# Kernel tuning notes

Hardware: AMD Instinct MI355X
Metric: run time of the kernel (lower is better)

Reference implementation:

```python
import jax, jax.numpy as jnp
import numpy as np

N_NODES = 50000
N_EDGES = 640000
IN_CH = 128
OUT_CH = 128
HID = 2 * OUT_CH  # 256


def _glorot(key, shape):
    fan_in, fan_out = shape
    lim = np.sqrt(6.0 / (fan_in + fan_out)).astype(np.float32)
    return jax.random.uniform(key, shape, jnp.float32, -lim, lim)


def setup_inputs() -> dict:
    key = jax.random.key(0)
    ks = jax.random.split(key, 8)
    x = jax.random.normal(ks[0], (N_NODES, IN_CH), jnp.float32)
    edge_index = jax.random.randint(ks[1], (2, N_EDGES), 0, N_NODES, jnp.int64)
    # SAGEConv layer 1: lin_l (neighbor branch, with bias), lin_r (root branch, no bias)
    w1_l = _glorot(ks[2], (IN_CH, HID))
    b1_l = jnp.zeros((HID,), jnp.float32)
    w1_r = _glorot(ks[3], (IN_CH, HID))
    # SAGEConv layer 2
    w2_l = _glorot(ks[4], (HID, OUT_CH))
    b2_l = jnp.zeros((OUT_CH,), jnp.float32)
    w2_r = _glorot(ks[5], (HID, OUT_CH))
    return {"x": x, "edge_index": edge_index,
            "w1_l": w1_l, "b1_l": b1_l, "w1_r": w1_r,
            "w2_l": w2_l, "b2_l": b2_l, "w2_r": w2_r}


def _sage_conv(x, src, dst, w_l, b_l, w_r):
    # mean aggregation of source-node features onto destination nodes
    msgs = x[src]                                       # [E, C] gather
    agg = jax.ops.segment_sum(msgs, dst, num_segments=N_NODES)  # [N, C]
    cnt = jax.ops.segment_sum(jnp.ones((src.shape[0],), x.dtype), dst,
                              num_segments=N_NODES)     # [N]
    mean = agg / jnp.maximum(cnt, 1.0)[:, None]
    # out = lin_l(mean_neighbors) + lin_r(x_root)
    return mean @ w_l + b_l + x @ w_r


def reference(x, edge_index, w1_l, b1_l, w1_r, w2_l, b2_l, w2_r):
    src, dst = edge_index[0], edge_index[1]
    h = _sage_conv(x, src, dst, w1_l, b1_l, w1_r)
    h = jax.nn.relu(h)
    return _sage_conv(h, src, dst, w2_l, b2_l, w2_r)
```

## Files before the change

### kernel.cpp

```cpp
#include <hip/hip_runtime.h>

#define N_NODES 50000
#define N_EDGES 640000
#define IN_CH 128
#define OUT_CH 128
#define HID 256
#define M_PAD 50048
#define NBLK ((N_NODES + 255) / 256)

typedef unsigned int uint;
typedef unsigned short ushort;

__device__ __forceinline__ ushort f2b(float f) {
    uint u = __float_as_uint(f);
    u += 0x7FFFu + ((u >> 16) & 1u);
    return (ushort)(u >> 16);
}
__device__ __forceinline__ float b2f_lo(uint u) { return __uint_as_float(u << 16); }
__device__ __forceinline__ float b2f_hi(uint u) { return __uint_as_float(u & 0xFFFF0000u); }
__device__ __forceinline__ uint packb(float lo, float hi) {
    return (uint)f2b(lo) | ((uint)f2b(hi) << 16);
}

__device__ __forceinline__ void gload_lds16(const ushort* g, ushort* l) {
    __builtin_amdgcn_global_load_lds(
        (const __attribute__((address_space(1))) void*)g,
        (__attribute__((address_space(3))) void*)l, 16, 0, 0);
}

__global__ __launch_bounds__(256) void count_deg(const int* __restrict__ dst,
                                                 int* __restrict__ deg) {
    int e = blockIdx.x * blockDim.x + threadIdx.x;
    if (e < N_EDGES) atomicAdd(&deg[dst[e]], 1);
}

__global__ __launch_bounds__(256) void block_sums(const int* __restrict__ deg,
                                                  int* __restrict__ bsum) {
    __shared__ int tmp[256];
    int i = blockIdx.x * 256 + threadIdx.x;
    tmp[threadIdx.x] = (i < N_NODES) ? deg[i] : 0;
    __syncthreads();
    for (int off = 128; off > 0; off >>= 1) {
        if (threadIdx.x < off) tmp[threadIdx.x] += tmp[threadIdx.x + off];
        __syncthreads();
    }
    if (threadIdx.x == 0) bsum[blockIdx.x] = tmp[0];
}

__global__ __launch_bounds__(256) void scan_bsums(int* __restrict__ bsum,
                                                  int* __restrict__ rowptr) {
    __shared__ int tmp[256];
    int i = threadIdx.x;
    int v = (i < NBLK) ? bsum[i] : 0;
    tmp[i] = v;
    __syncthreads();
    for (int off = 1; off < 256; off <<= 1) {
        int t = (i >= off) ? tmp[i - off] : 0;
        __syncthreads();
        tmp[i] += t;
        __syncthreads();
    }
    if (i < NBLK) bsum[i] = tmp[i] - v;
    if (i == 0) rowptr[N_NODES] = N_EDGES;
}

__global__ __launch_bounds__(256) void scan_final(const int* __restrict__ deg,
                                                  const int* __restrict__ bsum,
                                                  int* __restrict__ rowptr) {
    __shared__ int tmp[256];
    int i = blockIdx.x * 256 + threadIdx.x;
    int v = (i < N_NODES) ? deg[i] : 0;
    tmp[threadIdx.x] = v;
    __syncthreads();
    for (int off = 1; off < 256; off <<= 1) {
        int t = (threadIdx.x >= off) ? tmp[threadIdx.x - off] : 0;
        __syncthreads();
        tmp[threadIdx.x] += t;
        __syncthreads();
    }
    if (i < N_NODES) rowptr[i] = bsum[blockIdx.x] + tmp[threadIdx.x] - v;
}

__global__ __launch_bounds__(256) void fill_csr(const int* __restrict__ src,
                                                const int* __restrict__ dst,
                                                const int* __restrict__ rowptr,
                                                int* __restrict__ cursor,
                                                int* __restrict__ col) {
    int e = blockIdx.x * blockDim.x + threadIdx.x;
    if (e >= N_EDGES) return;
    int d = dst[e];
    int p = atomicAdd(&cursor[d], 1);
    col[rowptr[d] + p] = src[e];
}

__global__ __launch_bounds__(256) void cast_all(
    const float* __restrict__ x, const float* __restrict__ w1l,
    const float* __restrict__ w1r, const float* __restrict__ w2l,
    const float* __restrict__ w2r, ushort* __restrict__ xcat,
    ushort* __restrict__ w1f, ushort* __restrict__ w2f) {
    int id = blockIdx.x * 256 + threadIdx.x;
    if (id < 800000) {
        long long base = (long long)id * 8;
        float4 a = *(const float4*)(x + base);
        float4 b = *(const float4*)(x + base + 4);
        uint4 o;
        o.x = packb(a.x, a.y);
        o.y = packb(a.z, a.w);
        o.z = packb(b.x, b.y);
        o.w = packb(b.z, b.w);
        int row = id >> 4;
        int c = id & 15;
        ((uint4*)xcat)[(size_t)row * 32 + 16 + c] = o;
    } else if (id < 865536) {
        int i = id - 800000;
        int n0 = i >> 12, kk = (i >> 9) & 7, lane = (i >> 3) & 63, j = i & 7;
        int n = n0 * 16 + (lane & 15);
        int k = kk * 32 + (lane >> 4) * 8 + j;
        float v = (k < 128) ? w1l[k * 256 + n] : w1r[(k - 128) * 256 + n];
        w1f[i] = f2b(v);
    } else {
        int i = id - 865536;
        int n0 = i >> 12, kk = (i >> 9) & 7, lane = (i >> 3) & 63, j = i & 7;
        int n = n0 * 16 + (lane & 15);
        int k = kk * 32 + (lane >> 4) * 8 + j;
        float v = (n < 128) ? w2l[k * 128 + n] : w2r[k * 128 + (n - 128)];
        w2f[i] = f2b(v);
    }
}

__global__ __launch_bounds__(256) void aggregate_mean1(
    const int* __restrict__ rowptr, const int* __restrict__ col,
    ushort* __restrict__ xcat) {
    int t = blockIdx.x * 256 + threadIdx.x;
    int node = t >> 5;
    int q = t & 15;
    int half = (t >> 4) & 1;
    if (node >= N_NODES) return;
    int beg = rowptr[node], end = rowptr[node + 1];
    float acc[8] = {0.f, 0.f, 0.f, 0.f, 0.f, 0.f, 0.f, 0.f};
    const uint4* f4 = (const uint4*)xcat;
    for (int j = beg + half; j < end; j += 2) {
        int s = col[j];
        uint4 v = f4[(size_t)s * 32 + 16 + q];
        acc[0] += b2f_lo(v.x); acc[1] += b2f_hi(v.x);
        acc[2] += b2f_lo(v.y); acc[3] += b2f_hi(v.y);
        acc[4] += b2f_lo(v.z); acc[5] += b2f_hi(v.z);
        acc[6] += b2f_lo(v.w); acc[7] += b2f_hi(v.w);
    }
#pragma unroll
    for (int k = 0; k < 8; ++k) acc[k] += __shfl_xor(acc[k], 16);
    if (half == 0) {
        float inv = 1.0f / fmaxf((float)(end - beg), 1.0f);
        uint4 o;
        o.x = packb(acc[0] * inv, acc[1] * inv);
        o.y = packb(acc[2] * inv, acc[3] * inv);
        o.z = packb(acc[4] * inv, acc[5] * inv);
        o.w = packb(acc[6] * inv, acc[7] * inv);
        ((uint4*)xcat)[(size_t)node * 32 + q] = o;
    }
}

__global__ __launch_bounds__(256) void combine2(
    const ushort* __restrict__ hw, const int* __restrict__ rowptr,
    const int* __restrict__ col, const float* __restrict__ bias,
    float* __restrict__ out) {
    int t = blockIdx.x * 256 + threadIdx.x;
    int node = t >> 5;
    int q = t & 15;
    int half = (t >> 4) & 1;
    if (node >= N_NODES) return;
    int beg = rowptr[node], end = rowptr[node + 1];
    float acc[8] = {0.f, 0.f, 0.f, 0.f, 0.f, 0.f, 0.f, 0.f};
    const uint4* f4 = (const uint4*)hw;
    for (int j = beg + half; j < end; j += 2) {
        int s = col[j];
        uint4 v = f4[(size_t)s * 32 + q];
        acc[0] += b2f_lo(v.x); acc[1] += b2f_hi(v.x);
        acc[2] += b2f_lo(v.y); acc[3] += b2f_hi(v.y);
        acc[4] += b2f_lo(v.z); acc[5] += b2f_hi(v.z);
        acc[6] += b2f_lo(v.w); acc[7] += b2f_hi(v.w);
    }
#pragma unroll
    for (int k = 0; k < 8; ++k) acc[k] += __shfl_xor(acc[k], 16);
    if (half == 0) {
        float inv = 1.0f / fmaxf((float)(end - beg), 1.0f);
        uint4 r = f4[(size_t)node * 32 + 16 + q];
        float4 b0 = *(const float4*)(bias + q * 8);
        float4 b1 = *(const float4*)(bias + q * 8 + 4);
        float4 o0, o1;
        o0.x = acc[0] * inv + b2f_lo(r.x) + b0.x;
        o0.y = acc[1] * inv + b2f_hi(r.x) + b0.y;
        o0.z = acc[2] * inv + b2f_lo(r.y) + b0.z;
        o0.w = acc[3] * inv + b2f_hi(r.y) + b0.w;
        o1.x = acc[4] * inv + b2f_lo(r.z) + b1.x;
        o1.y = acc[5] * inv + b2f_hi(r.z) + b1.y;
        o1.z = acc[6] * inv + b2f_lo(r.w) + b1.z;
        o1.w = acc[7] * inv + b2f_hi(r.w) + b1.w;
        *(float4*)(out + (size_t)node * 128 + q * 8) = o0;
        *(float4*)(out + (size_t)node * 128 + q * 8 + 4) = o1;
    }
}

using bf16x8 = __attribute__((ext_vector_type(8))) short;
using f32x4  = __attribute__((ext_vector_type(4))) float;

__global__ __launch_bounds__(256) void fused_gemm(
    const ushort* __restrict__ A, const ushort* __restrict__ w1f,
    const ushort* __restrict__ w2f, const float* __restrict__ b1,
    ushort* __restrict__ hw) {
    __shared__ alignas(16) ushort As[64 * 128];
    __shared__ alignas(16) ushort hS[64 * 256];

    const int tid = threadIdx.x;
    const int lane = tid & 63;
    const int wave = tid >> 6;
    const int quad = lane >> 4;
    const int l16 = lane & 15;
    const int bm = blockIdx.x * 64;

    const int srow = tid >> 4;
    const int sslot = tid & 15;

    f32x4 acc[4][4];
#pragma unroll
    for (int rt = 0; rt < 4; ++rt)
#pragma unroll
        for (int ct = 0; ct < 4; ++ct) acc[rt][ct] = (f32x4){0.f, 0.f, 0.f, 0.f};

#pragma unroll
    for (int kh = 0; kh < 2; ++kh) {
#pragma unroll
        for (int r = 0; r < 4; ++r) {
            int rl = r * 16 + srow;
            int c = sslot ^ (rl & 7);
            const ushort* g = A + (size_t)(bm + rl) * 256 + kh * 128 + c * 8;
            gload_lds16(g, &As[rl * 128 + sslot * 8]);
        }
        __syncthreads();
#pragma unroll
        for (int kk = 0; kk < 128; kk += 32) {
            bf16x8 af[4];
#pragma unroll
            for (int rt = 0; rt < 4; ++rt) {
                int row = rt * 16 + l16;
                int slot = ((kk >> 3) + quad) ^ (row & 7);
                af[rt] = *(const bf16x8*)&As[row * 128 + slot * 8];
            }
            int kkidx = kh * 4 + (kk >> 5);
#pragma unroll
            for (int ct = 0; ct < 4; ++ct) {
                int n0 = wave * 4 + ct;
                bf16x8 bf = *(const bf16x8*)(w1f + (((size_t)(n0 * 8 + kkidx) * 64 + lane) << 3));
                acc[0][ct] = __builtin_amdgcn_mfma_f32_16x16x32_bf16(af[0], bf, acc[0][ct], 0, 0, 0);
                acc[1][ct] = __builtin_amdgcn_mfma_f32_16x16x32_bf16(af[1], bf, acc[1][ct], 0, 0, 0);
                acc[2][ct] = __builtin_amdgcn_mfma_f32_16x16x32_bf16(af[2], bf, acc[2][ct], 0, 0, 0);
                acc[3][ct] = __builtin_amdgcn_mfma_f32_16x16x32_bf16(af[3], bf, acc[3][ct], 0, 0, 0);
            }
        }
        __syncthreads();
    }

#pragma unroll
    for (int ct = 0; ct < 4; ++ct) {
        int colg = wave * 64 + ct * 16 + l16;
        float bv = b1[colg];
        int c_chunk = colg >> 3;
        int off = colg & 7;
#pragma unroll
        for (int rt = 0; rt < 4; ++rt) {
#pragma unroll
            for (int reg = 0; reg < 4; ++reg) {
                int row = rt * 16 + quad * 4 + reg;
                float v = fmaxf(acc[rt][ct][reg] + bv, 0.0f);
                int slot = c_chunk ^ (row & 7);
                hS[row * 256 + slot * 8 + off] = f2b(v);
            }
        }
    }
    __syncthreads();

#pragma unroll
    for (int rt = 0; rt < 4; ++rt)
#pragma unroll
        for (int ct = 0; ct < 4; ++ct) acc[rt][ct] = (f32x4){0.f, 0.f, 0.f, 0.f};

#pragma unroll
    for (int kk = 0; kk < 256; kk += 32) {
        bf16x8 af[4];
#pragma unroll
        for (int rt = 0; rt < 4; ++rt) {
            int row = rt * 16 + l16;
            int slot = ((kk >> 3) + quad) ^ (row & 7);
            af[rt] = *(const bf16x8*)&hS[row * 256 + slot * 8];
        }
        int kkidx = kk >> 5;
#pragma unroll
        for (int ct = 0; ct < 4; ++ct) {
            int n0 = wave * 4 + ct;
            bf16x8 bf = *(const bf16x8*)(w2f + (((size_t)(n0 * 8 + kkidx) * 64 + lane) << 3));
            acc[0][ct] = __builtin_amdgcn_mfma_f32_16x16x32_bf16(af[0], bf, acc[0][ct], 0, 0, 0);
            acc[1][ct] = __builtin_amdgcn_mfma_f32_16x16x32_bf16(af[1], bf, acc[1][ct], 0, 0, 0);
            acc[2][ct] = __builtin_amdgcn_mfma_f32_16x16x32_bf16(af[2], bf, acc[2][ct], 0, 0, 0);
            acc[3][ct] = __builtin_amdgcn_mfma_f32_16x16x32_bf16(af[3], bf, acc[3][ct], 0, 0, 0);
        }
    }
    __syncthreads();

#pragma unroll
    for (int ct = 0; ct < 4; ++ct) {
        int colg = wave * 64 + ct * 16 + l16;
        int c_chunk = colg >> 3;
        int off = colg & 7;
#pragma unroll
        for (int rt = 0; rt < 4; ++rt) {
#pragma unroll
            for (int reg = 0; reg < 4; ++reg) {
                int row = rt * 16 + quad * 4 + reg;
                int slot = c_chunk ^ (row & 7);
                hS[row * 256 + slot * 8 + off] = f2b(acc[rt][ct][reg]);
            }
        }
    }
    __syncthreads();
#pragma unroll
    for (int r = 0; r < 8; ++r) {
        int row = r * 8 + (tid >> 5);
        int chunk = tid & 31;
        int slot = chunk ^ (row & 7);
        uint4 v = *(const uint4*)&hS[row * 256 + slot * 8];
        *(uint4*)(hw + (size_t)(bm + row) * 256 + chunk * 8) = v;
    }
}

extern "C" void kernel_launch(void* const* d_in, const int* in_sizes, int n_in,
                              void* d_out, int out_size, void* d_ws, size_t ws_size,
                              hipStream_t stream) {
    const float* x    = (const float*)d_in[0];
    const int*   ei   = (const int*)d_in[1];
    const float* w1_l = (const float*)d_in[2];
    const float* b1_l = (const float*)d_in[3];
    const float* w1_r = (const float*)d_in[4];
    const float* w2_l = (const float*)d_in[5];
    const float* b2_l = (const float*)d_in[6];
    const float* w2_r = (const float*)d_in[7];
    float* out = (float*)d_out;

    const int* src = ei;
    const int* dst = ei + N_EDGES;

    int* deg    = (int*)d_ws;
    int* cursor = deg + N_NODES;
    int* rowptr = cursor + N_NODES;
    int* bsum   = rowptr + (N_NODES + 1);
    int* col    = bsum + NBLK;
    size_t int_bytes = (size_t)(2 * N_NODES + (N_NODES + 1) + NBLK + N_EDGES) * 4;
    size_t ofs = (int_bytes + 15) & ~(size_t)15;
    ushort* xcat = (ushort*)((char*)d_ws + ofs);
    ushort* hw   = xcat + (size_t)M_PAD * HID;
    ushort* w1f  = hw + (size_t)M_PAD * HID;
    ushort* w2f  = w1f + HID * HID;

    hipMemsetAsync(deg, 0, 2 * (size_t)N_NODES * sizeof(int), stream);

    count_deg<<<(N_EDGES + 255) / 256, 256, 0, stream>>>(dst, deg);
    block_sums<<<NBLK, 256, 0, stream>>>(deg, bsum);
    scan_bsums<<<1, 256, 0, stream>>>(bsum, rowptr);
    scan_final<<<NBLK, 256, 0, stream>>>(deg, bsum, rowptr);
    fill_csr<<<(N_EDGES + 255) / 256, 256, 0, stream>>>(src, dst, rowptr, cursor, col);

    cast_all<<<3637, 256, 0, stream>>>(x, w1_l, w1_r, w2_l, w2_r, xcat, w1f, w2f);

    aggregate_mean1<<<N_NODES * 32 / 256, 256, 0, stream>>>(rowptr, col, xcat);
    fused_gemm<<<M_PAD / 64, 256, 0, stream>>>(xcat, w1f, w2f, b1_l, hw);
    combine2<<<N_NODES * 32 / 256, 256, 0, stream>>>(hw, rowptr, col, b2_l, out);
}
```

Before: 279.8 us.

## Shrink GEMM tile to 32 rows with single LDS buffer; unroll gather loops

```diff
diff --git a/kernel.cpp b/kernel.cpp
--- a/kernel.cpp
+++ b/kernel.cpp
@@ -139,9 +139,18 @@
     int beg = rowptr[node], end = rowptr[node + 1];
     float acc[8] = {0.f, 0.f, 0.f, 0.f, 0.f, 0.f, 0.f, 0.f};
     const uint4* f4 = (const uint4*)xcat;
-    for (int j = beg + half; j < end; j += 2) {
-        int s = col[j];
-        uint4 v = f4[(size_t)s * 32 + 16 + q];
+    int j = beg + half;
+    for (; j + 2 < end; j += 4) {
+        int s0 = col[j], s1 = col[j + 2];
+        uint4 v0 = f4[(size_t)s0 * 32 + 16 + q];
+        uint4 v1 = f4[(size_t)s1 * 32 + 16 + q];
+        acc[0] += b2f_lo(v0.x) + b2f_lo(v1.x); acc[1] += b2f_hi(v0.x) + b2f_hi(v1.x);
+        acc[2] += b2f_lo(v0.y) + b2f_lo(v1.y); acc[3] += b2f_hi(v0.y) + b2f_hi(v1.y);
+        acc[4] += b2f_lo(v0.z) + b2f_lo(v1.z); acc[5] += b2f_hi(v0.z) + b2f_hi(v1.z);
+        acc[6] += b2f_lo(v0.w) + b2f_lo(v1.w); acc[7] += b2f_hi(v0.w) + b2f_hi(v1.w);
+    }
+    if (j < end) {
+        uint4 v = f4[(size_t)col[j] * 32 + 16 + q];
         acc[0] += b2f_lo(v.x); acc[1] += b2f_hi(v.x);
         acc[2] += b2f_lo(v.y); acc[3] += b2f_hi(v.y);
         acc[4] += b2f_lo(v.z); acc[5] += b2f_hi(v.z);
@@ -172,9 +181,18 @@
     int beg = rowptr[node], end = rowptr[node + 1];
     float acc[8] = {0.f, 0.f, 0.f, 0.f, 0.f, 0.f, 0.f, 0.f};
     const uint4* f4 = (const uint4*)hw;
-    for (int j = beg + half; j < end; j += 2) {
-        int s = col[j];
-        uint4 v = f4[(size_t)s * 32 + q];
+    int j = beg + half;
+    for (; j + 2 < end; j += 4) {
+        int s0 = col[j], s1 = col[j + 2];
+        uint4 v0 = f4[(size_t)s0 * 32 + q];
+        uint4 v1 = f4[(size_t)s1 * 32 + q];
+        acc[0] += b2f_lo(v0.x) + b2f_lo(v1.x); acc[1] += b2f_hi(v0.x) + b2f_hi(v1.x);
+        acc[2] += b2f_lo(v0.y) + b2f_lo(v1.y); acc[3] += b2f_hi(v0.y) + b2f_hi(v1.y);
+        acc[4] += b2f_lo(v0.z) + b2f_lo(v1.z); acc[5] += b2f_hi(v0.z) + b2f_hi(v1.z);
+        acc[6] += b2f_lo(v0.w) + b2f_lo(v1.w); acc[7] += b2f_hi(v0.w) + b2f_hi(v1.w);
+    }
+    if (j < end) {
+        uint4 v = f4[(size_t)col[j] * 32 + q];
         acc[0] += b2f_lo(v.x); acc[1] += b2f_hi(v.x);
         acc[2] += b2f_lo(v.y); acc[3] += b2f_hi(v.y);
         acc[4] += b2f_lo(v.z); acc[5] += b2f_hi(v.z);
@@ -208,90 +226,84 @@
     const ushort* __restrict__ A, const ushort* __restrict__ w1f,
     const ushort* __restrict__ w2f, const float* __restrict__ b1,
     ushort* __restrict__ hw) {
-    __shared__ alignas(16) ushort As[64 * 128];
-    __shared__ alignas(16) ushort hS[64 * 256];
+    __shared__ alignas(16) ushort tile[32 * 256];
 
     const int tid = threadIdx.x;
     const int lane = tid & 63;
     const int wave = tid >> 6;
     const int quad = lane >> 4;
     const int l16 = lane & 15;
-    const int bm = blockIdx.x * 64;
-
-    const int srow = tid >> 4;
-    const int sslot = tid & 15;
-
-    f32x4 acc[4][4];
-#pragma unroll
-    for (int rt = 0; rt < 4; ++rt)
+    const int bm = blockIdx.x * 32;
+
+    f32x4 acc[2][4];
+#pragma unroll
+    for (int rt = 0; rt < 2; ++rt)
 #pragma unroll
         for (int ct = 0; ct < 4; ++ct) acc[rt][ct] = (f32x4){0.f, 0.f, 0.f, 0.f};
 
 #pragma unroll
-    for (int kh = 0; kh < 2; ++kh) {
-#pragma unroll
-        for (int r = 0; r < 4; ++r) {
-            int rl = r * 16 + srow;
-            int c = sslot ^ (rl & 7);
-            const ushort* g = A + (size_t)(bm + rl) * 256 + kh * 128 + c * 8;
-            gload_lds16(g, &As[rl * 128 + sslot * 8]);
-        }
-        __syncthreads();
-#pragma unroll
-        for (int kk = 0; kk < 128; kk += 32) {
-            bf16x8 af[4];
-#pragma unroll
-            for (int rt = 0; rt < 4; ++rt) {
-                int row = rt * 16 + l16;
-                int slot = ((kk >> 3) + quad) ^ (row & 7);
-                af[rt] = *(const bf16x8*)&As[row * 128 + slot * 8];
-            }
-            int kkidx = kh * 4 + (kk >> 5);
-#pragma unroll
-            for (int ct = 0; ct < 4; ++ct) {
-                int n0 = wave * 4 + ct;
-                bf16x8 bf = *(const bf16x8*)(w1f + (((size_t)(n0 * 8 + kkidx) * 64 + lane) << 3));
-                acc[0][ct] = __builtin_amdgcn_mfma_f32_16x16x32_bf16(af[0], bf, acc[0][ct], 0, 0, 0);
-                acc[1][ct] = __builtin_amdgcn_mfma_f32_16x16x32_bf16(af[1], bf, acc[1][ct], 0, 0, 0);
-                acc[2][ct] = __builtin_amdgcn_mfma_f32_16x16x32_bf16(af[2], bf, acc[2][ct], 0, 0, 0);
-                acc[3][ct] = __builtin_amdgcn_mfma_f32_16x16x32_bf16(af[3], bf, acc[3][ct], 0, 0, 0);
-            }
-        }
-        __syncthreads();
-    }
+    for (int r = 0; r < 4; ++r) {
+        int row = (r * 4 + wave) * 2 + (lane >> 5);
+        int c = lane & 31;
+        int src = (c & 24) | ((c & 7) ^ (row & 7));
+        const ushort* g = A + (size_t)(bm + row) * 256 + src * 8;
+        gload_lds16(g, &tile[row * 256 + c * 8]);
+    }
+    __syncthreads();
+
+#pragma unroll
+    for (int kk = 0; kk < 256; kk += 32) {
+        bf16x8 af[2];
+#pragma unroll
+        for (int rt = 0; rt < 2; ++rt) {
+            int row = rt * 16 + l16;
+            int c = (kk >> 3) + quad;
+            int slot = (c & 24) | ((c & 7) ^ (row & 7));
+            af[rt] = *(const bf16x8*)&tile[row * 256 + slot * 8];
+        }
+        int kkidx = kk >> 5;
+#pragma unroll
+        for (int ct = 0; ct < 4; ++ct) {
+            int n0 = wave * 4 + ct;
+            bf16x8 bf = *(const bf16x8*)(w1f + (((size_t)(n0 * 8 + kkidx) * 64 + lane) << 3));
+            acc[0][ct] = __builtin_amdgcn_mfma_f32_16x16x32_bf16(af[0], bf, acc[0][ct], 0, 0, 0);
+            acc[1][ct] = __builtin_amdgcn_mfma_f32_16x16x32_bf16(af[1], bf, acc[1][ct], 0, 0, 0);
+        }
+    }
+    __syncthreads();
 
 #pragma unroll
     for (int ct = 0; ct < 4; ++ct) {
         int colg = wave * 64 + ct * 16 + l16;
         float bv = b1[colg];
-        int c_chunk = colg >> 3;
+        int c = colg >> 3;
         int off = colg & 7;
 #pragma unroll
-        for (int rt = 0; rt < 4; ++rt) {
+        for (int rt = 0; rt < 2; ++rt) {
 #pragma unroll
             for (int reg = 0; reg < 4; ++reg) {
                 int row = rt * 16 + quad * 4 + reg;
-                float v = fmaxf(acc[rt][ct][reg] + bv, 0.0f);
-                int slot = c_chunk ^ (row & 7);
-                hS[row * 256 + slot * 8 + off] = f2b(v);
+                int slot = (c & 24) | ((c & 7) ^ (row & 7));
+                tile[row * 256 + slot * 8 + off] = f2b(fmaxf(acc[rt][ct][reg] + bv, 0.0f));
             }
         }
     }
     __syncthreads();
 
 #pragma unroll
-    for (int rt = 0; rt < 4; ++rt)
+    for (int rt = 0; rt < 2; ++rt)
 #pragma unroll
         for (int ct = 0; ct < 4; ++ct) acc[rt][ct] = (f32x4){0.f, 0.f, 0.f, 0.f};
 
 #pragma unroll
     for (int kk = 0; kk < 256; kk += 32) {
-        bf16x8 af[4];
-#pragma unroll
-        for (int rt = 0; rt < 4; ++rt) {
+        bf16x8 af[2];
+#pragma unroll
+        for (int rt = 0; rt < 2; ++rt) {
             int row = rt * 16 + l16;
-            int slot = ((kk >> 3) + quad) ^ (row & 7);
-            af[rt] = *(const bf16x8*)&hS[row * 256 + slot * 8];
+            int c = (kk >> 3) + quad;
+            int slot = (c & 24) | ((c & 7) ^ (row & 7));
+            af[rt] = *(const bf16x8*)&tile[row * 256 + slot * 8];
         }
         int kkidx = kk >> 5;
 #pragma unroll
@@ -300,8 +312,6 @@
             bf16x8 bf = *(const bf16x8*)(w2f + (((size_t)(n0 * 8 + kkidx) * 64 + lane) << 3));
             acc[0][ct] = __builtin_amdgcn_mfma_f32_16x16x32_bf16(af[0], bf, acc[0][ct], 0, 0, 0);
             acc[1][ct] = __builtin_amdgcn_mfma_f32_16x16x32_bf16(af[1], bf, acc[1][ct], 0, 0, 0);
-            acc[2][ct] = __builtin_amdgcn_mfma_f32_16x16x32_bf16(af[2], bf, acc[2][ct], 0, 0, 0);
-            acc[3][ct] = __builtin_amdgcn_mfma_f32_16x16x32_bf16(af[3], bf, acc[3][ct], 0, 0, 0);
         }
     }
     __syncthreads();
@@ -309,26 +319,26 @@
 #pragma unroll
     for (int ct = 0; ct < 4; ++ct) {
         int colg = wave * 64 + ct * 16 + l16;
-        int c_chunk = colg >> 3;
+        int c = colg >> 3;
         int off = colg & 7;
 #pragma unroll
-        for (int rt = 0; rt < 4; ++rt) {
+        for (int rt = 0; rt < 2; ++rt) {
 #pragma unroll
             for (int reg = 0; reg < 4; ++reg) {
                 int row = rt * 16 + quad * 4 + reg;
-                int slot = c_chunk ^ (row & 7);
-                hS[row * 256 + slot * 8 + off] = f2b(acc[rt][ct][reg]);
+                int slot = (c & 24) | ((c & 7) ^ (row & 7));
+                tile[row * 256 + slot * 8 + off] = f2b(acc[rt][ct][reg]);
             }
         }
     }
     __syncthreads();
 #pragma unroll
-    for (int r = 0; r < 8; ++r) {
-        int row = r * 8 + (tid >> 5);
-        int chunk = tid & 31;
-        int slot = chunk ^ (row & 7);
-        uint4 v = *(const uint4*)&hS[row * 256 + slot * 8];
-        *(uint4*)(hw + (size_t)(bm + row) * 256 + chunk * 8) = v;
+    for (int r = 0; r < 4; ++r) {
+        int row = (r * 4 + wave) * 2 + (lane >> 5);
+        int c = lane & 31;
+        int slot = (c & 24) | ((c & 7) ^ (row & 7));
+        uint4 v = *(const uint4*)&tile[row * 256 + slot * 8];
+        *(uint4*)(hw + (size_t)(bm + row) * 256 + c * 8) = v;
     }
 }
 
@@ -371,6 +381,6 @@
     cast_all<<<3637, 256, 0, stream>>>(x, w1_l, w1_r, w2_l, w2_r, xcat, w1f, w2f);
 
     aggregate_mean1<<<N_NODES * 32 / 256, 256, 0, stream>>>(rowptr, col, xcat);
-    fused_gemm<<<M_PAD / 64, 256, 0, stream>>>(xcat, w1f, w2f, b1_l, hw);
+    fused_gemm<<<M_PAD / 32, 256, 0, stream>>>(xcat, w1f, w2f, b1_l, hw);
     combine2<<<N_NODES * 32 / 256, 256, 0, stream>>>(hw, rowptr, col, b2_l, out);
 }
```

Result: faster. 272.3 us (-2.7%).
